# Kernel tuning notes

Measured on AMD Instinct MI355X. Metric: run time of the kernel, lower is better.

The kernel has to match this reference:

```python
import jax, jax.numpy as jnp
import numpy as np

BETA = 0.5
TEMPERATURE = 1.0
IGNORE_INDEX = -100
BT, H, V = 2048, 2048, 32000


def setup_inputs() -> dict:
    key = jax.random.key(0)
    k1, k2, k3, k4, k5 = jax.random.split(key, 5)
    return {
        "student_input": jax.random.normal(k1, (BT, H), dtype=jnp.float32),
        "student_weight": jax.random.normal(k2, (V, H), dtype=jnp.float32) * 0.02,
        "teacher_input": jax.random.normal(k3, (BT, H), dtype=jnp.float32),
        "teacher_weight": jax.random.normal(k4, (V, H), dtype=jnp.float32) * 0.02,
        "labels": jax.random.randint(k5, (BT,), 0, V, dtype=jnp.int64),
    }


def reference(student_input, student_weight, teacher_input, teacher_weight, labels):
    # logits = x @ W^T, scaled by temperature, then log-softmax (computed in fp32)
    s_logits = jnp.einsum("bh,vh->bv", student_input, student_weight).astype(jnp.float32)
    t_logits = jnp.einsum("bh,vh->bv", teacher_input, teacher_weight).astype(jnp.float32)
    s_lp = jax.nn.log_softmax(s_logits / TEMPERATURE, axis=-1)  # log Q, (BT, V)
    t_lp = jax.nn.log_softmax(t_logits / TEMPERATURE, axis=-1)  # log P, (BT, V)
    Q = jnp.exp(s_lp)
    P = jnp.exp(t_lp)
    # generalized JSD: M = beta*P + (1-beta)*Q
    log_m = jnp.log(BETA * P + (1.0 - BETA) * Q)
    per_row = jnp.sum(BETA * P * (t_lp - log_m) + (1.0 - BETA) * Q * (s_lp - log_m), axis=-1)  # (BT,)
    valid = (labels != IGNORE_INDEX)
    n_non_ignore = jnp.maximum(jnp.sum(valid), 1).astype(jnp.float32)
    loss = jnp.sum(jnp.where(valid, per_row, 0.0)) / n_non_ignore
    return loss
```

## Files before the change

### kernel.cpp

```cpp
#include <hip/hip_runtime.h>
#include <stdint.h>

#define BT 2048
#define H  2048
#define V  32000

typedef __attribute__((ext_vector_type(8))) short short8;
typedef __attribute__((ext_vector_type(4))) float f32x4;

__device__ inline unsigned short f2bf(float x) {
  unsigned int u = __float_as_uint(x);
  u += 0x7FFFu + ((u >> 16) & 1u);
  return (unsigned short)(u >> 16);
}

__global__ void zero_accum(float* accum) {
  accum[0] = 0.0f;
  ((unsigned int*)accum)[1] = 0u;
}

__global__ __launch_bounds__(256) void cvt_kernel(const float* __restrict__ src,
                                                  unsigned short* __restrict__ dst,
                                                  int n8) {
  int i = blockIdx.x * blockDim.x + threadIdx.x;
  if (i >= n8) return;
  const float4* s = (const float4*)src;
  float4 a = s[2 * i];
  float4 b = s[2 * i + 1];
  union { unsigned short us[8]; uint4 v; } o;
  o.us[0] = f2bf(a.x); o.us[1] = f2bf(a.y); o.us[2] = f2bf(a.z); o.us[3] = f2bf(a.w);
  o.us[4] = f2bf(b.x); o.us[5] = f2bf(b.y); o.us[6] = f2bf(b.z); o.us[7] = f2bf(b.w);
  ((uint4*)dst)[i] = o.v;
}

#define BM 128
#define BN 128
#define BK 32

__global__ __launch_bounds__(256) void gemm_bt(const unsigned short* __restrict__ A0,
                                               const unsigned short* __restrict__ B0,
                                               const unsigned short* __restrict__ A1,
                                               const unsigned short* __restrict__ B1,
                                               unsigned short* __restrict__ C0,
                                               unsigned short* __restrict__ C1) {
  const int z = blockIdx.z;
  const unsigned short* A = z ? A1 : A0;
  const unsigned short* B = z ? B1 : B0;
  unsigned short* C = z ? C1 : C0;

  const int m0 = blockIdx.x * BM;
  const int n0 = blockIdx.y * BN;

  __shared__ alignas(16) unsigned short lA[BM * BK];
  __shared__ alignas(16) unsigned short lB[BN * BK];

  const int tid  = threadIdx.x;
  const int lane = tid & 63;
  const int w    = tid >> 6;
  const int wm   = w & 1;
  const int wn   = w >> 1;

  f32x4 acc[4][4];
  #pragma unroll
  for (int i = 0; i < 4; i++)
    #pragma unroll
    for (int j = 0; j < 4; j++)
      acc[i][j] = (f32x4){0.f, 0.f, 0.f, 0.f};

  const int q  = lane >> 4;
  const int l4 = lane & 15;

  for (int k0 = 0; k0 < H; k0 += BK) {
    #pragma unroll
    for (int i = 0; i < 2; i++) {
      int basec = (i * 4 + w) * 64;
      int c     = basec + lane;
      int row   = c >> 2;
      int cq    = c & 3;
      const unsigned short* ga = A + (size_t)(m0 + row) * H + k0 + cq * 8;
      const unsigned short* gb = B + (size_t)(n0 + row) * H + k0 + cq * 8;
      __builtin_amdgcn_global_load_lds(
          (const __attribute__((address_space(1))) unsigned int*)ga,
          (__attribute__((address_space(3))) unsigned int*)&lA[basec * 8], 16, 0, 0);
      __builtin_amdgcn_global_load_lds(
          (const __attribute__((address_space(1))) unsigned int*)gb,
          (__attribute__((address_space(3))) unsigned int*)&lB[basec * 8], 16, 0, 0);
    }
    __syncthreads();

    short8 af[4], bf[4];
    #pragma unroll
    for (int mi = 0; mi < 4; mi++) {
      int M = wm * 64 + mi * 16 + l4;
      af[mi] = *(const short8*)&lA[(M * 4 + q) * 8];
    }
    #pragma unroll
    for (int ni = 0; ni < 4; ni++) {
      int N = wn * 64 + ni * 16 + l4;
      bf[ni] = *(const short8*)&lB[(N * 4 + q) * 8];
    }

    #pragma unroll
    for (int mi = 0; mi < 4; mi++)
      #pragma unroll
      for (int ni = 0; ni < 4; ni++)
        acc[mi][ni] = __builtin_amdgcn_mfma_f32_16x16x32_bf16(af[mi], bf[ni], acc[mi][ni], 0, 0, 0);

    __syncthreads();
  }

  #pragma unroll
  for (int mi = 0; mi < 4; mi++)
    #pragma unroll
    for (int ni = 0; ni < 4; ni++)
      #pragma unroll
      for (int r = 0; r < 4; r++) {
        int gr = m0 + wm * 64 + mi * 16 + q * 4 + r;
        int gc = n0 + wn * 64 + ni * 16 + l4;
        C[(size_t)gr * V + gc] = f2bf(acc[mi][ni][r]);
      }
}

__device__ inline void unpack8(uint4 v, float* f) {
  f[0] = __uint_as_float(v.x << 16);
  f[1] = __uint_as_float(v.x & 0xFFFF0000u);
  f[2] = __uint_as_float(v.y << 16);
  f[3] = __uint_as_float(v.y & 0xFFFF0000u);
  f[4] = __uint_as_float(v.z << 16);
  f[5] = __uint_as_float(v.z & 0xFFFF0000u);
  f[6] = __uint_as_float(v.w << 16);
  f[7] = __uint_as_float(v.w & 0xFFFF0000u);
}

__device__ inline float blk_max(float v, float* red, int tid) {
  #pragma unroll
  for (int o = 32; o > 0; o >>= 1) v = fmaxf(v, __shfl_xor(v, o, 64));
  __syncthreads();
  if ((tid & 63) == 0) red[tid >> 6] = v;
  __syncthreads();
  return fmaxf(fmaxf(red[0], red[1]), fmaxf(red[2], red[3]));
}

__device__ inline float blk_sum(float v, float* red, int tid) {
  #pragma unroll
  for (int o = 32; o > 0; o >>= 1) v += __shfl_xor(v, o, 64);
  __syncthreads();
  if ((tid & 63) == 0) red[tid >> 6] = v;
  __syncthreads();
  return (red[0] + red[1]) + (red[2] + red[3]);
}

__global__ __launch_bounds__(256) void jsd_kernel(const unsigned short* __restrict__ Slog,
                                                  const unsigned short* __restrict__ Tlog,
                                                  const long long* __restrict__ labels,
                                                  float* __restrict__ accum) {
  const int r   = blockIdx.x;
  const int tid = threadIdx.x;
  __shared__ float red[4];

  const uint4* s4 = (const uint4*)(Slog + (size_t)r * V);
  const uint4* t4 = (const uint4*)(Tlog + (size_t)r * V);
  const int NC = V / 8;

  float smax = -1e30f, tmax = -1e30f;
  for (int c = tid; c < NC; c += 256) {
    uint4 sv = s4[c], tv = t4[c];
    float fs[8], ft[8];
    unpack8(sv, fs); unpack8(tv, ft);
    #pragma unroll
    for (int j = 0; j < 8; j++) {
      smax = fmaxf(smax, fs[j]);
      tmax = fmaxf(tmax, ft[j]);
    }
  }
  smax = blk_max(smax, red, tid);
  tmax = blk_max(tmax, red, tid);

  float ssum = 0.f, tsum = 0.f;
  for (int c = tid; c < NC; c += 256) {
    uint4 sv = s4[c], tv = t4[c];
    float fs[8], ft[8];
    unpack8(sv, fs); unpack8(tv, ft);
    #pragma unroll
    for (int j = 0; j < 8; j++) {
      ssum += __expf(fs[j] - smax);
      tsum += __expf(ft[j] - tmax);
    }
  }
  ssum = blk_sum(ssum, red, tid);
  tsum = blk_sum(tsum, red, tid);
  float slse = smax + __logf(ssum);
  float tlse = tmax + __logf(tsum);

  float loss = 0.f;
  for (int c = tid; c < NC; c += 256) {
    uint4 sv = s4[c], tv = t4[c];
    float fs[8], ft[8];
    unpack8(sv, fs); unpack8(tv, ft);
    #pragma unroll
    for (int j = 0; j < 8; j++) {
      float sl = fs[j] - slse;
      float tl = ft[j] - tlse;
      float qv = __expf(sl);
      float pv = __expf(tl);
      float m  = 0.5f * (pv + qv);
      float lm = __logf(m);
      loss += 0.5f * (pv * (tl - lm) + qv * (sl - lm));
    }
  }
  loss = blk_sum(loss, red, tid);

  if (tid == 0) {
    long long lab = labels[r];
    if (lab != -100LL) {
      atomicAdd(&accum[0], loss);
      atomicAdd((unsigned int*)&accum[1], 1u);
    }
  }
}

__global__ void finalize(const float* __restrict__ accum, float* __restrict__ out) {
  float cnt = (float)((const unsigned int*)accum)[1];
  out[0] = accum[0] / fmaxf(cnt, 1.0f);
}

extern "C" void kernel_launch(void* const* d_in, const int* in_sizes, int n_in,
                              void* d_out, int out_size, void* d_ws, size_t ws_size,
                              hipStream_t stream) {
  const float* s_in = (const float*)d_in[0];
  const float* s_w  = (const float*)d_in[1];
  const float* t_in = (const float*)d_in[2];
  const float* t_w  = (const float*)d_in[3];
  const long long* labels = (const long long*)d_in[4];
  float* out = (float*)d_out;

  char* ws = (char*)d_ws;
  size_t off = 0;
  auto take = [&](size_t bytes) -> char* {
    char* p = ws + off;
    off += (bytes + 255) & ~(size_t)255;
    return p;
  };
  unsigned short* sw_bf = (unsigned short*)take((size_t)V * H * 2);
  unsigned short* tw_bf = (unsigned short*)take((size_t)V * H * 2);
  unsigned short* si_bf = (unsigned short*)take((size_t)BT * H * 2);
  unsigned short* ti_bf = (unsigned short*)take((size_t)BT * H * 2);
  unsigned short* slog  = (unsigned short*)take((size_t)BT * V * 2);
  unsigned short* tlog  = (unsigned short*)take((size_t)BT * V * 2);
  float* accum = (float*)take(256);
  if (off > ws_size) return;

  zero_accum<<<dim3(1), dim3(1), 0, stream>>>(accum);

  const int nW8 = (V * H) / 8;
  const int nI8 = (BT * H) / 8;
  cvt_kernel<<<dim3((nW8 + 255) / 256), dim3(256), 0, stream>>>(s_w, sw_bf, nW8);
  cvt_kernel<<<dim3((nW8 + 255) / 256), dim3(256), 0, stream>>>(t_w, tw_bf, nW8);
  cvt_kernel<<<dim3((nI8 + 255) / 256), dim3(256), 0, stream>>>(s_in, si_bf, nI8);
  cvt_kernel<<<dim3((nI8 + 255) / 256), dim3(256), 0, stream>>>(t_in, ti_bf, nI8);

  gemm_bt<<<dim3(BT / BM, V / BN, 2), dim3(256), 0, stream>>>(si_bf, sw_bf, ti_bf, tw_bf, slog, tlog);

  jsd_kernel<<<dim3(BT), dim3(256), 0, stream>>>(slog, tlog, labels, accum);

  finalize<<<dim3(1), dim3(1), 0, stream>>>(accum, out);
}
```

Baseline: 1.366 ms.

## Rewrite GEMM with 256x256 tiles, 4-stage LDS pipeline, and online softmax

The bf16 GEMM moves to 256x256 tiles with 512 threads. It uses a four-buffer LDS ring fed by async global-to-LDS loads, swizzled LDS addressing, explicit waitcnt/barrier scheduling and setprio around the MFMA blocks, so global loads overlap compute. The JSD kernel merges its max and sum-exp passes into one online-softmax pass, removing one full read of both logit matrices. The gains are higher arithmetic intensity and fewer LDS stalls, at the cost of much more LDS per block, higher register pressure from 32 accumulators per lane, and fragile hand-written synchronization.

```diff
diff --git a/kernel.cpp b/kernel.cpp
--- a/kernel.cpp
+++ b/kernel.cpp
@@ -33,91 +33,132 @@
   ((uint4*)dst)[i] = o.v;
 }
 
-#define BM 128
-#define BN 128
-#define BK 32
-
-__global__ __launch_bounds__(256) void gemm_bt(const unsigned short* __restrict__ A0,
-                                               const unsigned short* __restrict__ B0,
-                                               const unsigned short* __restrict__ A1,
-                                               const unsigned short* __restrict__ B1,
-                                               unsigned short* __restrict__ C0,
-                                               unsigned short* __restrict__ C1) {
+#define GBM 256
+#define GBN 256
+#define GBK 32
+#define NKT (H / GBK)
+
+
+#define GLL(gp, lp) __builtin_amdgcn_global_load_lds( \
+    (const __attribute__((address_space(1))) unsigned int*)(gp), \
+    (__attribute__((address_space(3))) unsigned int*)(lp), 16, 0, 0)
+
+__global__ __launch_bounds__(512, 2) void gemm_bt(const unsigned short* __restrict__ A0,
+                                                  const unsigned short* __restrict__ B0,
+                                                  const unsigned short* __restrict__ A1,
+                                                  const unsigned short* __restrict__ B1,
+                                                  unsigned short* __restrict__ C0,
+                                                  unsigned short* __restrict__ C1) {
   const int z = blockIdx.z;
-  const unsigned short* A = z ? A1 : A0;
-  const unsigned short* B = z ? B1 : B0;
+  const unsigned short* Amat = z ? A1 : A0;
+  const unsigned short* Bmat = z ? B1 : B0;
   unsigned short* C = z ? C1 : C0;
 
-  const int m0 = blockIdx.x * BM;
-  const int n0 = blockIdx.y * BN;
-
-  __shared__ alignas(16) unsigned short lA[BM * BK];
-  __shared__ alignas(16) unsigned short lB[BN * BK];
+  const int m0 = blockIdx.x * GBM;
+  const int n0 = blockIdx.y * GBN;
+
+  __shared__ alignas(16) unsigned short lA[4][8192];
+  __shared__ alignas(16) unsigned short lB[4][8192];
 
   const int tid  = threadIdx.x;
   const int lane = tid & 63;
   const int w    = tid >> 6;
-  const int wm   = w & 1;
-  const int wn   = w >> 1;
-
-  f32x4 acc[4][4];
-  #pragma unroll
-  for (int i = 0; i < 4; i++)
+  const int wm   = w >> 2;
+  const int wn   = w & 3;
+  const int l4   = lane & 15;
+  const int q    = lane >> 4;
+
+  const unsigned short* ga[2];
+  const unsigned short* gb[2];
+  #pragma unroll
+  for (int j = 0; j < 2; j++) {
+    int p   = tid + j * 512;
+    int pr  = p >> 3;
+    int s0  = (p & 7) ^ ((pr & 3) << 1);
+    int row = (pr << 1) | (s0 & 1);
+    int cc  = s0 >> 1;
+    ga[j] = Amat + (size_t)(m0 + row) * H + cc * 8;
+    gb[j] = Bmat + (size_t)(n0 + row) * H + cc * 8;
+  }
+
+  const int s0f   = ((q << 1) | (l4 & 1)) ^ (l4 & 6);
+  const int Abase = (wm * 64 + (l4 >> 1)) * 64 + s0f * 8;
+  const int Bbase = (wn * 32 + (l4 >> 1)) * 64 + s0f * 8;
+
+  f32x4 acc[8][4];
+  #pragma unroll
+  for (int i = 0; i < 8; i++)
     #pragma unroll
     for (int j = 0; j < 4; j++)
       acc[i][j] = (f32x4){0.f, 0.f, 0.f, 0.f};
 
-  const int q  = lane >> 4;
-  const int l4 = lane & 15;
-
-  for (int k0 = 0; k0 < H; k0 += BK) {
-    #pragma unroll
-    for (int i = 0; i < 2; i++) {
-      int basec = (i * 4 + w) * 64;
-      int c     = basec + lane;
-      int row   = c >> 2;
-      int cq    = c & 3;
-      const unsigned short* ga = A + (size_t)(m0 + row) * H + k0 + cq * 8;
-      const unsigned short* gb = B + (size_t)(n0 + row) * H + k0 + cq * 8;
-      __builtin_amdgcn_global_load_lds(
-          (const __attribute__((address_space(1))) unsigned int*)ga,
-          (__attribute__((address_space(3))) unsigned int*)&lA[basec * 8], 16, 0, 0);
-      __builtin_amdgcn_global_load_lds(
-          (const __attribute__((address_space(1))) unsigned int*)gb,
-          (__attribute__((address_space(3))) unsigned int*)&lB[basec * 8], 16, 0, 0);
-    }
-    __syncthreads();
+  #pragma unroll
+  for (int t = 0; t < 3; t++) {
+    GLL(ga[0] + t * GBK, &lA[t][w * 512]);
+    GLL(ga[1] + t * GBK, &lA[t][w * 512 + 4096]);
+    GLL(gb[0] + t * GBK, &lB[t][w * 512]);
+    GLL(gb[1] + t * GBK, &lB[t][w * 512 + 4096]);
+  }
+  asm volatile("s_waitcnt vmcnt(8)" ::: "memory");
+  __builtin_amdgcn_s_barrier();
+
+  for (int t = 0; t < NKT; ++t) {
+    const int cur = t & 3;
+    const bool st = (t + 3) < NKT;
+    const int  sb = (t + 3) & 3;
 
     short8 af[4], bf[4];
     #pragma unroll
-    for (int mi = 0; mi < 4; mi++) {
-      int M = wm * 64 + mi * 16 + l4;
-      af[mi] = *(const short8*)&lA[(M * 4 + q) * 8];
-    }
-    #pragma unroll
-    for (int ni = 0; ni < 4; ni++) {
-      int N = wn * 64 + ni * 16 + l4;
-      bf[ni] = *(const short8*)&lB[(N * 4 + q) * 8];
-    }
-
-    #pragma unroll
-    for (int mi = 0; mi < 4; mi++)
+    for (int mf = 0; mf < 4; mf++) af[mf] = *(const short8*)&lA[cur][Abase + mf * 512];
+    #pragma unroll
+    for (int nf = 0; nf < 4; nf++) bf[nf] = *(const short8*)&lB[cur][Bbase + nf * 512];
+    if (st) {
+      GLL(ga[0] + (t + 3) * GBK, &lA[sb][w * 512]);
+      GLL(ga[1] + (t + 3) * GBK, &lA[sb][w * 512 + 4096]);
+    }
+    __builtin_amdgcn_s_barrier();
+    asm volatile("s_waitcnt lgkmcnt(0)" ::: "memory");
+    __builtin_amdgcn_s_setprio(1);
+    #pragma unroll
+    for (int mf = 0; mf < 4; mf++)
       #pragma unroll
-      for (int ni = 0; ni < 4; ni++)
-        acc[mi][ni] = __builtin_amdgcn_mfma_f32_16x16x32_bf16(af[mi], bf[ni], acc[mi][ni], 0, 0, 0);
-
-    __syncthreads();
-  }
-
-  #pragma unroll
-  for (int mi = 0; mi < 4; mi++)
-    #pragma unroll
-    for (int ni = 0; ni < 4; ni++)
+      for (int nf = 0; nf < 4; nf++)
+        acc[mf][nf] = __builtin_amdgcn_mfma_f32_16x16x32_bf16(af[mf], bf[nf], acc[mf][nf], 0, 0, 0);
+    __builtin_amdgcn_s_setprio(0);
+    __builtin_amdgcn_s_barrier();
+
+    short8 ag[4];
+    #pragma unroll
+    for (int mf = 0; mf < 4; mf++) ag[mf] = *(const short8*)&lA[cur][Abase + (mf + 4) * 512];
+    if (st) {
+      GLL(gb[0] + (t + 3) * GBK, &lB[sb][w * 512]);
+      GLL(gb[1] + (t + 3) * GBK, &lB[sb][w * 512 + 4096]);
+    }
+    __builtin_amdgcn_s_barrier();
+    asm volatile("s_waitcnt lgkmcnt(0)" ::: "memory");
+    __builtin_amdgcn_s_setprio(1);
+    #pragma unroll
+    for (int mf = 0; mf < 4; mf++)
+      #pragma unroll
+      for (int nf = 0; nf < 4; nf++)
+        acc[mf + 4][nf] = __builtin_amdgcn_mfma_f32_16x16x32_bf16(ag[mf], bf[nf], acc[mf + 4][nf], 0, 0, 0);
+    __builtin_amdgcn_s_setprio(0);
+
+    if (t < NKT - 3)       asm volatile("s_waitcnt vmcnt(8)" ::: "memory");
+    else if (t == NKT - 3) asm volatile("s_waitcnt vmcnt(4)" ::: "memory");
+    else                   asm volatile("s_waitcnt vmcnt(0)" ::: "memory");
+    __builtin_amdgcn_s_barrier();
+  }
+
+  #pragma unroll
+  for (int mf = 0; mf < 8; mf++)
+    #pragma unroll
+    for (int nf = 0; nf < 4; nf++)
       #pragma unroll
       for (int r = 0; r < 4; r++) {
-        int gr = m0 + wm * 64 + mi * 16 + q * 4 + r;
-        int gc = n0 + wn * 64 + ni * 16 + l4;
-        C[(size_t)gr * V + gc] = f2bf(acc[mi][ni][r]);
+        int gr = m0 + wm * 128 + mf * 16 + q * 4 + r;
+        int gc = n0 + wn * 64 + nf * 16 + l4;
+        C[(size_t)gr * V + gc] = f2bf(acc[mf][nf][r]);
       }
 }
 
@@ -162,35 +203,30 @@
   const uint4* t4 = (const uint4*)(Tlog + (size_t)r * V);
   const int NC = V / 8;
 
-  float smax = -1e30f, tmax = -1e30f;
+  float sm = -1e30f, ss = 0.f, tm = -1e30f, ts = 0.f;
   for (int c = tid; c < NC; c += 256) {
     uint4 sv = s4[c], tv = t4[c];
     float fs[8], ft[8];
     unpack8(sv, fs); unpack8(tv, ft);
+    float lms = fs[0], lmt = ft[0];
+    #pragma unroll
+    for (int j = 1; j < 8; j++) { lms = fmaxf(lms, fs[j]); lmt = fmaxf(lmt, ft[j]); }
+    if (lms > sm) { ss *= __expf(sm - lms); sm = lms; }
+    if (lmt > tm) { ts *= __expf(tm - lmt); tm = lmt; }
     #pragma unroll
     for (int j = 0; j < 8; j++) {
-      smax = fmaxf(smax, fs[j]);
-      tmax = fmaxf(tmax, ft[j]);
-    }
-  }
-  smax = blk_max(smax, red, tid);
-  tmax = blk_max(tmax, red, tid);
-
-  float ssum = 0.f, tsum = 0.f;
-  for (int c = tid; c < NC; c += 256) {
-    uint4 sv = s4[c], tv = t4[c];
-    float fs[8], ft[8];
-    unpack8(sv, fs); unpack8(tv, ft);
-    #pragma unroll
-    for (int j = 0; j < 8; j++) {
-      ssum += __expf(fs[j] - smax);
-      tsum += __expf(ft[j] - tmax);
-    }
-  }
-  ssum = blk_sum(ssum, red, tid);
-  tsum = blk_sum(tsum, red, tid);
-  float slse = smax + __logf(ssum);
-  float tlse = tmax + __logf(tsum);
+      ss += __expf(fs[j] - sm);
+      ts += __expf(ft[j] - tm);
+    }
+  }
+  float SM = blk_max(sm, red, tid);
+  ss *= __expf(sm - SM);
+  float SS = blk_sum(ss, red, tid);
+  float TM = blk_max(tm, red, tid);
+  ts *= __expf(tm - TM);
+  float TS = blk_sum(ts, red, tid);
+  float slse = SM + __logf(SS);
+  float tlse = TM + __logf(TS);
 
   float loss = 0.f;
   for (int c = tid; c < NC; c += 256) {
@@ -259,7 +295,7 @@
   cvt_kernel<<<dim3((nI8 + 255) / 256), dim3(256), 0, stream>>>(s_in, si_bf, nI8);
   cvt_kernel<<<dim3((nI8 + 255) / 256), dim3(256), 0, stream>>>(t_in, ti_bf, nI8);
 
-  gemm_bt<<<dim3(BT / BM, V / BN, 2), dim3(256), 0, stream>>>(si_bf, sw_bf, ti_bf, tw_bf, slog, tlog);
+  gemm_bt<<<dim3(BT / GBM, V / GBN, 2), dim3(512), 0, stream>>>(si_bf, sw_bf, ti_bf, tw_bf, slog, tlog);
 
   jsd_kernel<<<dim3(BT), dim3(256), 0, stream>>>(slog, tlog, labels, accum);
 
```

Measured after the change: 1.271 ms. -7.0%, faster.
